# Kernel optimization log

Measured on AMD Instinct MI355X. Metric: run time of the kernel, lower is better.

Reference implementation:

```python
import jax, jax.numpy as jnp
import numpy as np

IN_CH = 32
HID = 2 * IN_CH          # 64
MASK_CH = 8 * 27         # 216


def conv3d(x, w, b, replicate_pad):
    # x: [B,C,D,H,W], w: [O,I,kd,kh,kw]
    if replicate_pad:
        x = jnp.pad(x, ((0, 0), (0, 0), (1, 1), (1, 1), (1, 1)), mode='edge')
    y = jax.lax.conv_general_dilated(
        x, w, window_strides=(1, 1, 1), padding='VALID',
        dimension_numbers=('NCDHW', 'OIDHW', 'NCDHW'))
    return y + b[None, :, None, None, None]


def unfold27(x):
    # replicate-padded 3x3x3 neighborhoods -> [B,C,D,H,W,27], n = kd*9+kh*3+kw
    B, C, D, H, W = x.shape
    xp = jnp.pad(x, ((0, 0), (0, 0), (1, 1), (1, 1), (1, 1)), mode='edge')
    patches = [xp[:, :, dz:dz + D, dy:dy + H, dx:dx + W]
               for dz in range(3) for dy in range(3) for dx in range(3)]
    return jnp.stack(patches, axis=-1)


def setup_inputs() -> dict:
    key = jax.random.key(0)
    ks = jax.random.split(key, 6)
    B, C, D, H, W = 1, IN_CH, 48, 48, 48
    x = jax.random.normal(ks[0], (B, C, D, H, W), dtype=jnp.float32)
    features = jax.random.normal(ks[1], (B, IN_CH, D, H, W), dtype=jnp.float32)
    # Conv(in, 2*in, k=3, replicate pad) ; Conv(2*in, 8*27, k=1, zeros pad)
    w1 = jax.random.normal(ks[2], (HID, IN_CH, 3, 3, 3), dtype=jnp.float32) * (1.0 / np.sqrt(IN_CH * 27))
    b1 = jnp.zeros((HID,), dtype=jnp.float32)
    w2 = jax.random.normal(ks[3], (MASK_CH, HID, 1, 1, 1), dtype=jnp.float32) * (1.0 / np.sqrt(HID))
    b2 = jnp.zeros((MASK_CH,), dtype=jnp.float32)
    return {"x": x, "features": features, "w1": w1, "b1": b1, "w2": w2, "b2": b2}


def reference(x, features, w1, b1, w2, b2):
    B, C, D, H, W = x.shape
    # mask network: Conv3 (replicate) -> SiLU -> Conv1 (zeros)
    h = jax.nn.silu(conv3d(features, w1, b1, replicate_pad=True))
    m = conv3d(h, w2, b2, replicate_pad=False)          # [B,216,D,H,W]
    # view(B,1,2,2,2,27,D,H,W).permute(0,1,6,2,7,3,8,4,5) -> [B,D,2,H,2,W,2,27]
    m = m.reshape(B, 2, 2, 2, 27, D, H, W)
    m = jnp.transpose(m, (0, 5, 1, 6, 2, 7, 3, 4))      # b d i h j w k n
    m = jax.nn.softmax(m, axis=-1)
    xu = unfold27(x)                                    # [B,C,D,H,W,27]
    # convex combination: contract over the 27 taps (batched small matmul)
    out = jnp.einsum('bdihjwkn,bcdhwn->bcdihjwk', m, xu)
    return out.reshape(B, C, 2 * D, 2 * H, 2 * W)
```

## Files before the change

kernel.cpp:

```cpp
#include <hip/hip_runtime.h>
#include <math.h>

#define NVOX 110592

typedef _Float16 f16x8 __attribute__((ext_vector_type(8)));
typedef _Float16 f16x4 __attribute__((ext_vector_type(4)));
typedef _Float16 f16x2 __attribute__((ext_vector_type(2)));
typedef float    f32x4 __attribute__((ext_vector_type(4)));

__device__ __forceinline__ void fmas4(float4& a, const float4& xv, float p) {
    a.x = fmaf(xv.x, p, a.x);
    a.y = fmaf(xv.y, p, a.y);
    a.z = fmaf(xv.z, p, a.z);
    a.w = fmaf(xv.w, p, a.w);
}
__device__ __forceinline__ float comp4(const float4& v, int j) {
    return j == 0 ? v.x : (j == 1 ? v.y : (j == 2 ? v.z : v.w));
}

__device__ __forceinline__ int xcd_swizzle(int bx, int nwg) {
    int chunk = nwg >> 3;
    return (bx & 7) * chunk + (bx >> 3);
}

__global__ void k_prep(const float* __restrict__ w1, const float* __restrict__ w2,
                       _Float16* __restrict__ w1h, _Float16* __restrict__ w2h) {
    int e = blockIdx.x * 256 + threadIdx.x;
    if (e < 64 * 32 * 27) {
        int oc = e / 864;
        int r = e - oc * 864;
        int ci = r / 27;
        int tap = r - ci * 27;
        w1h[oc * 864 + tap * 32 + ci] = (_Float16)w1[e];
    }
    int e2 = e - 55296;
    if (e2 >= 0 && e2 < 224 * 64) {
        int oc = e2 >> 6, k = e2 & 63;
        w2h[e2] = (oc < 216) ? (_Float16)w2[oc * 64 + k] : (_Float16)0.f;
    }
}

__global__ __launch_bounds__(256) void k_prepT(
    const float* __restrict__ feat, const float* __restrict__ x,
    _Float16* __restrict__ featT, _Float16* __restrict__ xT)
{
    __shared__ _Float16 tile[64 * 36];
    int bx = blockIdx.x;
    int which = bx >= 1728;
    int v0 = (which ? bx - 1728 : bx) * 64;
    const float* s = which ? x : feat;
    _Float16* dt = which ? xT : featT;
    int t = threadIdx.x;

    for (int i = t; i < 1024; i += 256) {
        int c2 = i >> 6, dv = i & 63;
        f16x2 v;
        v.x = (_Float16)s[(2 * c2) * NVOX + v0 + dv];
        v.y = (_Float16)s[(2 * c2 + 1) * NVOX + v0 + dv];
        *(f16x2*)(tile + dv * 36 + c2 * 2) = v;
    }
    __syncthreads();
    for (int i = t; i < 512; i += 256) {
        int dv = i >> 3, ch = i & 7;
        f16x4 v = *(const f16x4*)(tile + dv * 36 + ch * 4);
        *(f16x4*)(dt + (v0 + dv) * 32 + ch * 4) = v;
    }
}

__global__ __launch_bounds__(256, 4) void k_conv1(
    const _Float16* __restrict__ featT, const _Float16* __restrict__ w1h,
    const float* __restrict__ b1, _Float16* __restrict__ hout)
{
    __shared__ _Float16 flds[450 * 40];
    int bx = xcd_swizzle(blockIdx.x, gridDim.x);
    int d = bx / 48, hh = bx - d * 48;
    int t = threadIdx.x;

    for (int i = t; i < 1800; i += 256) {
        int col = i >> 2, chunk = i & 3;
        int dzdy = col / 50;
        int px = col - dzdy * 50;
        int dz = dzdy / 3, dy = dzdy - dz * 3;
        int zz = min(max(d + dz - 1, 0), 47);
        int yy = min(max(hh + dy - 1, 0), 47);
        int xx = min(max(px - 1, 0), 47);
        int vox = (zz * 48 + yy) * 48 + xx;
        *(f16x8*)(flds + col * 40 + chunk * 8) =
            *(const f16x8*)(featT + vox * 32 + chunk * 8);
    }
    __syncthreads();

    int wid = t >> 6;
    int lane = t & 63;
    int mcol = lane & 15;
    int q = lane >> 4;

    const _Float16* wbase = w1h + (wid * 16 + mcol) * 864 + q * 8;

    f32x4 acc0 = {0.f, 0.f, 0.f, 0.f};
    f32x4 acc1 = {0.f, 0.f, 0.f, 0.f};
    f32x4 acc2 = {0.f, 0.f, 0.f, 0.f};

#pragma unroll 3
    for (int dzdy = 0; dzdy < 9; ++dzdy) {
        const _Float16* brow = flds + (dzdy * 50 + mcol) * 40 + q * 8;
        const _Float16* wrow = wbase + dzdy * 96;
#pragma unroll
        for (int dx = 0; dx < 3; ++dx) {
            f16x8 av = *(const f16x8*)(wrow + dx * 32);
            const _Float16* bb = brow + dx * 40;
            f16x8 b0 = *(const f16x8*)(bb);
            f16x8 b1v = *(const f16x8*)(bb + 16 * 40);
            f16x8 b2v = *(const f16x8*)(bb + 32 * 40);
            acc0 = __builtin_amdgcn_mfma_f32_16x16x32_f16(av, b0, acc0, 0, 0, 0);
            acc1 = __builtin_amdgcn_mfma_f32_16x16x32_f16(av, b1v, acc1, 0, 0, 0);
            acc2 = __builtin_amdgcn_mfma_f32_16x16x32_f16(av, b2v, acc2, 0, 0, 0);
        }
    }

    __syncthreads();
    _Float16* transh = flds;
    float4 bv = ((const float4*)b1)[wid * 4 + q];
    {
        f32x4 accs[3] = {acc0, acc1, acc2};
#pragma unroll
        for (int p = 0; p < 3; ++p) {
            int px = p * 16 + mcol;
            f16x4 o;
            float s;
            s = accs[p][0] + bv.x; o.x = (_Float16)(s / (1.f + __expf(-s)));
            s = accs[p][1] + bv.y; o.y = (_Float16)(s / (1.f + __expf(-s)));
            s = accs[p][2] + bv.z; o.z = (_Float16)(s / (1.f + __expf(-s)));
            s = accs[p][3] + bv.w; o.w = (_Float16)(s / (1.f + __expf(-s)));
            *(f16x4*)(transh + px * 72 + wid * 16 + q * 4) = o;
        }
    }
    __syncthreads();
    for (int i = t; i < 384; i += 256) {
        int c = i & 7, px = i >> 3;
        f16x8 v = *(const f16x8*)(transh + px * 72 + c * 8);
        ((f16x8*)hout)[(bx * 48 + px) * 8 + c] = v;
    }
}

__global__ __launch_bounds__(256, 4) void k_fused(
    const _Float16* __restrict__ xT, const _Float16* __restrict__ hws,
    const _Float16* __restrict__ w2h, const float* __restrict__ b2,
    float* __restrict__ out)
{
    __shared__ float smem[10056];
    _Float16* hl = (_Float16*)(smem + 5376);
    _Float16* xh = (_Float16*)(smem + 5376);
    int bx = xcd_swizzle(blockIdx.x, gridDim.x);
    int d = bx / 96;
    int r = bx - d * 96;
    int hh = r >> 1;
    int w0 = (r & 1) * 24;
    int t = threadIdx.x;
    int vox0 = (d * 48 + hh) * 48 + w0;

    if (t < 192) {
        int vox = t >> 3, c = t & 7;
        *(f16x8*)(hl + vox * 72 + c * 8) = ((const f16x8*)hws)[(vox0 + vox) * 8 + c];
    } else {
        int i = t - 192;
        int vox = 24 + (i >> 3), c = i & 7;
        f16x8 z = {0, 0, 0, 0, 0, 0, 0, 0};
        *(f16x8*)(hl + vox * 72 + c * 8) = z;
    }
    __syncthreads();

    {
        int wid = t >> 6, lane = t & 63;
        int mcol = lane & 15, q = lane >> 4;
        for (int mt = wid; mt < 14; mt += 4) {
            float bias[4];
#pragma unroll
            for (int rr = 0; rr < 4; ++rr) {
                int oc = mt * 16 + q * 4 + rr;
                bias[rr] = (oc < 216) ? b2[oc] : 0.f;
            }
            f32x4 acc0 = {bias[0], bias[1], bias[2], bias[3]};
            f32x4 acc1 = acc0;
#pragma unroll
            for (int ks = 0; ks < 2; ++ks) {
                f16x8 av = *(const f16x8*)(w2h + (mt * 16 + mcol) * 64 + ks * 32 + q * 8);
                f16x8 bv0 = *(const f16x8*)(hl + mcol * 72 + ks * 32 + q * 8);
                f16x8 bv1 = *(const f16x8*)(hl + (16 + mcol) * 72 + ks * 32 + q * 8);
                acc0 = __builtin_amdgcn_mfma_f32_16x16x32_f16(av, bv0, acc0, 0, 0, 0);
                acc1 = __builtin_amdgcn_mfma_f32_16x16x32_f16(av, bv1, acc1, 0, 0, 0);
            }
#pragma unroll
            for (int rr = 0; rr < 4; ++rr) {
                int oc = mt * 16 + q * 4 + rr;
                if (oc < 216) {
                    int sub = oc / 27;
                    int n = oc - sub * 27;
                    smem[(sub * 24 + mcol) * 28 + n] = acc0[rr];
                    int vox1 = 16 + mcol;
                    if (vox1 < 24)
                        smem[(sub * 24 + vox1) * 28 + n] = acc1[rr];
                }
            }
        }
    }
    __syncthreads();

    for (int i = t; i < 936; i += 256) {
        int col = i >> 2, chunk = i & 3;
        int dzdy = col / 26;
        int px = col - dzdy * 26;
        int dz = dzdy / 3, dy = dzdy - dz * 3;
        int zz = min(max(d + dz - 1, 0), 47);
        int yy = min(max(hh + dy - 1, 0), 47);
        int xx = min(max(w0 + px - 1, 0), 47);
        int vox = (zz * 48 + yy) * 48 + xx;
        *(f16x8*)(xh + col * 40 + chunk * 8) =
            *(const f16x8*)(xT + vox * 32 + chunk * 8);
    }
    if (t < 192) {
        int sub = t / 24;
        int vox = t - sub * 24;
        float4* p4p = (float4*)(smem + (sub * 24 + vox) * 28);
        float4 v[7];
#pragma unroll
        for (int g = 0; g < 7; ++g) v[g] = p4p[g];
        float mx = fmaxf(fmaxf(v[6].x, v[6].y), v[6].z);
#pragma unroll
        for (int g = 0; g < 6; ++g)
            mx = fmaxf(mx, fmaxf(fmaxf(v[g].x, v[g].y), fmaxf(v[g].z, v[g].w)));
        float s = 0.f;
#pragma unroll
        for (int g = 0; g < 7; ++g) {
            v[g].x = __expf(v[g].x - mx);
            v[g].y = __expf(v[g].y - mx);
            v[g].z = __expf(v[g].z - mx);
            v[g].w = __expf(v[g].w - mx);
        }
        v[6].w = 0.f;
#pragma unroll
        for (int g = 0; g < 7; ++g) s += v[g].x + v[g].y + v[g].z + v[g].w;
        float inv = 1.f / s;
#pragma unroll
        for (int g = 0; g < 7; ++g) {
            v[g].x *= inv; v[g].y *= inv; v[g].z *= inv; v[g].w *= inv;
            p4p[g] = v[g];
        }
    }
    __syncthreads();

    float4* smem4 = (float4*)smem;
    int tx = t & 7, ty = t >> 3;
    int cq = ty & 7, sp = ty >> 3;
    float4 acc[2][3];
#pragma unroll
    for (int s = 0; s < 2; ++s)
#pragma unroll
        for (int wi = 0; wi < 3; ++wi)
            acc[s][wi] = make_float4(0.f, 0.f, 0.f, 0.f);

#pragma unroll
    for (int g = 0; g < 7; ++g) {
        float4 p4[2][3];
#pragma unroll
        for (int s = 0; s < 2; ++s)
#pragma unroll
            for (int wi = 0; wi < 3; ++wi)
                p4[s][wi] = smem4[((sp * 2 + s) * 24 + tx + wi * 8) * 7 + g];
#pragma unroll
        for (int j = 0; j < 4; ++j) {
            int n = g * 4 + j;
            if (n < 27) {
                int dz = n / 9;
                int rem = n - dz * 9;
                int dy = rem / 3, dx = rem - dy * 3;
#pragma unroll
                for (int wi = 0; wi < 3; ++wi) {
                    int col = (dz * 3 + dy) * 26 + tx + wi * 8 + dx;
                    f16x4 xr = *(const f16x4*)(xh + col * 40 + cq * 4);
                    float4 xv = make_float4((float)xr.x, (float)xr.y,
                                            (float)xr.z, (float)xr.w);
                    fmas4(acc[0][wi], xv, comp4(p4[0][wi], j));
                    fmas4(acc[1][wi], xv, comp4(p4[1][wi], j));
                }
            }
        }
    }

    int i_ = sp >> 1, j_ = sp & 1;
    int rowz = 2 * d + i_;
    int rowy = 2 * hh + j_;
#pragma unroll
    for (int wi = 0; wi < 3; ++wi) {
        int wg = w0 + tx + wi * 8;
#pragma unroll
        for (int cc = 0; cc < 4; ++cc) {
            int c = cq * 4 + cc;
            float2 v;
            v.x = comp4(acc[0][wi], cc);
            v.y = comp4(acc[1][wi], cc);
            *(float2*)(out + (((size_t)c * 96 + rowz) * 96 + rowy) * 96 + 2 * wg) = v;
        }
    }
}

extern "C" void kernel_launch(void* const* d_in, const int* in_sizes, int n_in,
                              void* d_out, int out_size, void* d_ws, size_t ws_size,
                              hipStream_t stream) {
    const float* x    = (const float*)d_in[0];
    const float* feat = (const float*)d_in[1];
    const float* w1   = (const float*)d_in[2];
    const float* b1   = (const float*)d_in[3];
    const float* w2   = (const float*)d_in[4];
    const float* b2   = (const float*)d_in[5];
    float* out = (float*)d_out;

    _Float16* w1h   = (_Float16*)d_ws;
    _Float16* w2h   = (_Float16*)((char*)d_ws + 110592);
    _Float16* featT = (_Float16*)((char*)d_ws + 139264);
    _Float16* xT    = (_Float16*)((char*)d_ws + 7217152);
    _Float16* hws   = (_Float16*)((char*)d_ws + 14295040);

    k_prep<<<272, 256, 0, stream>>>(w1, w2, w1h, w2h);
    k_prepT<<<3456, 256, 0, stream>>>(feat, x, featT, xT);
    k_conv1<<<2304, 256, 0, stream>>>(featT, w1h, b1, hws);
    k_fused<<<4608, 256, 0, stream>>>(xT, hws, w2h, b2, out);
}
```

Measured before the change: 258.9 us.

## Fuse conv1 with mask conv and softmax upsampling into one row kernel

```diff
diff --git a/kernel.cpp b/kernel.cpp
--- a/kernel.cpp
+++ b/kernel.cpp
@@ -23,34 +23,37 @@
     return (bx & 7) * chunk + (bx >> 3);
 }
 
-__global__ void k_prep(const float* __restrict__ w1, const float* __restrict__ w2,
-                       _Float16* __restrict__ w1h, _Float16* __restrict__ w2h) {
-    int e = blockIdx.x * 256 + threadIdx.x;
-    if (e < 64 * 32 * 27) {
-        int oc = e / 864;
-        int r = e - oc * 864;
-        int ci = r / 27;
-        int tap = r - ci * 27;
-        w1h[oc * 864 + tap * 32 + ci] = (_Float16)w1[e];
-    }
-    int e2 = e - 55296;
-    if (e2 >= 0 && e2 < 224 * 64) {
-        int oc = e2 >> 6, k = e2 & 63;
-        w2h[e2] = (oc < 216) ? (_Float16)w2[oc * 64 + k] : (_Float16)0.f;
-    }
-}
-
-__global__ __launch_bounds__(256) void k_prepT(
+__global__ __launch_bounds__(256) void k_prep(
     const float* __restrict__ feat, const float* __restrict__ x,
-    _Float16* __restrict__ featT, _Float16* __restrict__ xT)
+    const float* __restrict__ w1, const float* __restrict__ w2,
+    _Float16* __restrict__ featT, _Float16* __restrict__ xT,
+    _Float16* __restrict__ w1h, _Float16* __restrict__ w2h)
 {
     __shared__ _Float16 tile[64 * 36];
     int bx = blockIdx.x;
+    int t = threadIdx.x;
+
+    if (bx >= 3456) {
+        int e = (bx - 3456) * 256 + t;
+        if (e < 64 * 32 * 27) {
+            int oc = e / 864;
+            int r = e - oc * 864;
+            int ci = r / 27;
+            int tap = r - ci * 27;
+            w1h[oc * 864 + tap * 32 + ci] = (_Float16)w1[e];
+        }
+        int e2 = e - 55296;
+        if (e2 >= 0 && e2 < 224 * 64) {
+            int oc = e2 >> 6, k = e2 & 63;
+            w2h[e2] = (oc < 216) ? (_Float16)w2[oc * 64 + k] : (_Float16)0.f;
+        }
+        return;
+    }
+
     int which = bx >= 1728;
     int v0 = (which ? bx - 1728 : bx) * 64;
     const float* s = which ? x : feat;
     _Float16* dt = which ? xT : featT;
-    int t = threadIdx.x;
 
     for (int i = t; i < 1024; i += 256) {
         int c2 = i >> 6, dv = i & 63;
@@ -67,16 +70,22 @@
     }
 }
 
-__global__ __launch_bounds__(256, 4) void k_conv1(
-    const _Float16* __restrict__ featT, const _Float16* __restrict__ w1h,
-    const float* __restrict__ b1, _Float16* __restrict__ hout)
+__global__ __launch_bounds__(512, 4) void k_main(
+    const _Float16* __restrict__ featT, const _Float16* __restrict__ xT,
+    const _Float16* __restrict__ w1h, const float* __restrict__ b1,
+    const _Float16* __restrict__ w2h, const float* __restrict__ b2,
+    float* __restrict__ out)
 {
-    __shared__ _Float16 flds[450 * 40];
+    __shared__ float smem[19752];
+    float* mbuf = smem;
+    _Float16* X  = (_Float16*)(smem + 10752);
+    _Float16* hl = (_Float16*)(smem + 10752);
+
     int bx = xcd_swizzle(blockIdx.x, gridDim.x);
     int d = bx / 48, hh = bx - d * 48;
     int t = threadIdx.x;
 
-    for (int i = t; i < 1800; i += 256) {
+    for (int i = t; i < 1800; i += 512) {
         int col = i >> 2, chunk = i & 3;
         int dzdy = col / 50;
         int px = col - dzdy * 50;
@@ -85,7 +94,7 @@
         int yy = min(max(hh + dy - 1, 0), 47);
         int xx = min(max(px - 1, 0), 47);
         int vox = (zz * 48 + yy) * 48 + xx;
-        *(f16x8*)(flds + col * 40 + chunk * 8) =
+        *(f16x8*)(X + col * 40 + chunk * 8) =
             *(const f16x8*)(featT + vox * 32 + chunk * 8);
     }
     __syncthreads();
@@ -94,134 +103,99 @@
     int lane = t & 63;
     int mcol = lane & 15;
     int q = lane >> 4;
-
-    const _Float16* wbase = w1h + (wid * 16 + mcol) * 864 + q * 8;
-
-    f32x4 acc0 = {0.f, 0.f, 0.f, 0.f};
-    f32x4 acc1 = {0.f, 0.f, 0.f, 0.f};
-    f32x4 acc2 = {0.f, 0.f, 0.f, 0.f};
-
+    int ocs = wid & 3;
+
+    f32x4 c1a = {0.f, 0.f, 0.f, 0.f};
+    f32x4 c1b = {0.f, 0.f, 0.f, 0.f};
+    {
+        const _Float16* wbase = w1h + (ocs * 16 + mcol) * 864 + q * 8;
 #pragma unroll 3
-    for (int dzdy = 0; dzdy < 9; ++dzdy) {
-        const _Float16* brow = flds + (dzdy * 50 + mcol) * 40 + q * 8;
-        const _Float16* wrow = wbase + dzdy * 96;
-#pragma unroll
-        for (int dx = 0; dx < 3; ++dx) {
-            f16x8 av = *(const f16x8*)(wrow + dx * 32);
-            const _Float16* bb = brow + dx * 40;
-            f16x8 b0 = *(const f16x8*)(bb);
-            f16x8 b1v = *(const f16x8*)(bb + 16 * 40);
-            f16x8 b2v = *(const f16x8*)(bb + 32 * 40);
-            acc0 = __builtin_amdgcn_mfma_f32_16x16x32_f16(av, b0, acc0, 0, 0, 0);
-            acc1 = __builtin_amdgcn_mfma_f32_16x16x32_f16(av, b1v, acc1, 0, 0, 0);
-            acc2 = __builtin_amdgcn_mfma_f32_16x16x32_f16(av, b2v, acc2, 0, 0, 0);
-        }
-    }
-
-    __syncthreads();
-    _Float16* transh = flds;
-    float4 bv = ((const float4*)b1)[wid * 4 + q];
-    {
-        f32x4 accs[3] = {acc0, acc1, acc2};
-#pragma unroll
-        for (int p = 0; p < 3; ++p) {
-            int px = p * 16 + mcol;
-            f16x4 o;
-            float s;
-            s = accs[p][0] + bv.x; o.x = (_Float16)(s / (1.f + __expf(-s)));
-            s = accs[p][1] + bv.y; o.y = (_Float16)(s / (1.f + __expf(-s)));
-            s = accs[p][2] + bv.z; o.z = (_Float16)(s / (1.f + __expf(-s)));
-            s = accs[p][3] + bv.w; o.w = (_Float16)(s / (1.f + __expf(-s)));
-            *(f16x4*)(transh + px * 72 + wid * 16 + q * 4) = o;
-        }
-    }
-    __syncthreads();
-    for (int i = t; i < 384; i += 256) {
-        int c = i & 7, px = i >> 3;
-        f16x8 v = *(const f16x8*)(transh + px * 72 + c * 8);
-        ((f16x8*)hout)[(bx * 48 + px) * 8 + c] = v;
-    }
-}
-
-__global__ __launch_bounds__(256, 4) void k_fused(
-    const _Float16* __restrict__ xT, const _Float16* __restrict__ hws,
-    const _Float16* __restrict__ w2h, const float* __restrict__ b2,
-    float* __restrict__ out)
-{
-    __shared__ float smem[10056];
-    _Float16* hl = (_Float16*)(smem + 5376);
-    _Float16* xh = (_Float16*)(smem + 5376);
-    int bx = xcd_swizzle(blockIdx.x, gridDim.x);
-    int d = bx / 96;
-    int r = bx - d * 96;
-    int hh = r >> 1;
-    int w0 = (r & 1) * 24;
-    int t = threadIdx.x;
-    int vox0 = (d * 48 + hh) * 48 + w0;
-
-    if (t < 192) {
-        int vox = t >> 3, c = t & 7;
-        *(f16x8*)(hl + vox * 72 + c * 8) = ((const f16x8*)hws)[(vox0 + vox) * 8 + c];
-    } else {
-        int i = t - 192;
-        int vox = 24 + (i >> 3), c = i & 7;
-        f16x8 z = {0, 0, 0, 0, 0, 0, 0, 0};
-        *(f16x8*)(hl + vox * 72 + c * 8) = z;
-    }
-    __syncthreads();
-
-    {
-        int wid = t >> 6, lane = t & 63;
-        int mcol = lane & 15, q = lane >> 4;
-        for (int mt = wid; mt < 14; mt += 4) {
-            float bias[4];
-#pragma unroll
-            for (int rr = 0; rr < 4; ++rr) {
-                int oc = mt * 16 + q * 4 + rr;
-                bias[rr] = (oc < 216) ? b2[oc] : 0.f;
-            }
-            f32x4 acc0 = {bias[0], bias[1], bias[2], bias[3]};
-            f32x4 acc1 = acc0;
-#pragma unroll
-            for (int ks = 0; ks < 2; ++ks) {
-                f16x8 av = *(const f16x8*)(w2h + (mt * 16 + mcol) * 64 + ks * 32 + q * 8);
-                f16x8 bv0 = *(const f16x8*)(hl + mcol * 72 + ks * 32 + q * 8);
-                f16x8 bv1 = *(const f16x8*)(hl + (16 + mcol) * 72 + ks * 32 + q * 8);
-                acc0 = __builtin_amdgcn_mfma_f32_16x16x32_f16(av, bv0, acc0, 0, 0, 0);
-                acc1 = __builtin_amdgcn_mfma_f32_16x16x32_f16(av, bv1, acc1, 0, 0, 0);
-            }
-#pragma unroll
-            for (int rr = 0; rr < 4; ++rr) {
-                int oc = mt * 16 + q * 4 + rr;
-                if (oc < 216) {
-                    int sub = oc / 27;
-                    int n = oc - sub * 27;
-                    smem[(sub * 24 + mcol) * 28 + n] = acc0[rr];
-                    int vox1 = 16 + mcol;
-                    if (vox1 < 24)
-                        smem[(sub * 24 + vox1) * 28 + n] = acc1[rr];
+        for (int dzdy = 0; dzdy < 9; ++dzdy) {
+            const _Float16* brow = X + (dzdy * 50 + mcol) * 40 + q * 8;
+            const _Float16* wrow = wbase + dzdy * 96;
+#pragma unroll
+            for (int dx = 0; dx < 3; ++dx) {
+                f16x8 av = *(const f16x8*)(wrow + dx * 32);
+                const _Float16* bb = brow + dx * 40;
+                if (wid < 4) {
+                    f16x8 b0 = *(const f16x8*)(bb);
+                    f16x8 b2v = *(const f16x8*)(bb + 32 * 40);
+                    c1a = __builtin_amdgcn_mfma_f32_16x16x32_f16(av, b0, c1a, 0, 0, 0);
+                    c1b = __builtin_amdgcn_mfma_f32_16x16x32_f16(av, b2v, c1b, 0, 0, 0);
+                } else {
+                    f16x8 b1v = *(const f16x8*)(bb + 16 * 40);
+                    c1a = __builtin_amdgcn_mfma_f32_16x16x32_f16(av, b1v, c1a, 0, 0, 0);
                 }
             }
         }
     }
     __syncthreads();
 
-    for (int i = t; i < 936; i += 256) {
+    {
+        float4 bv = ((const float4*)b1)[ocs * 4 + q];
+        int pxb0 = (wid < 4) ? 0 : 1;
+        int px0 = pxb0 * 16 + mcol;
+        f16x4 o; float s;
+        s = c1a[0] + bv.x; o.x = (_Float16)(s / (1.f + __expf(-s)));
+        s = c1a[1] + bv.y; o.y = (_Float16)(s / (1.f + __expf(-s)));
+        s = c1a[2] + bv.z; o.z = (_Float16)(s / (1.f + __expf(-s)));
+        s = c1a[3] + bv.w; o.w = (_Float16)(s / (1.f + __expf(-s)));
+        *(f16x4*)(hl + px0 * 72 + ocs * 16 + q * 4) = o;
+        if (wid < 4) {
+            int px1 = 32 + mcol;
+            s = c1b[0] + bv.x; o.x = (_Float16)(s / (1.f + __expf(-s)));
+            s = c1b[1] + bv.y; o.y = (_Float16)(s / (1.f + __expf(-s)));
+            s = c1b[2] + bv.z; o.z = (_Float16)(s / (1.f + __expf(-s)));
+            s = c1b[3] + bv.w; o.w = (_Float16)(s / (1.f + __expf(-s)));
+            *(f16x4*)(hl + px1 * 72 + ocs * 16 + q * 4) = o;
+        }
+    }
+    __syncthreads();
+
+    for (int tt = wid; tt < 42; tt += 8) {
+        int mt = tt / 3, nt = tt - mt * 3;
+        float bias[4];
+#pragma unroll
+        for (int rr = 0; rr < 4; ++rr) {
+            int oc = mt * 16 + q * 4 + rr;
+            bias[rr] = (oc < 216) ? b2[oc] : 0.f;
+        }
+        f32x4 acc = {bias[0], bias[1], bias[2], bias[3]};
+#pragma unroll
+        for (int ks = 0; ks < 2; ++ks) {
+            f16x8 av = *(const f16x8*)(w2h + (mt * 16 + mcol) * 64 + ks * 32 + q * 8);
+            f16x8 bv = *(const f16x8*)(hl + (nt * 16 + mcol) * 72 + ks * 32 + q * 8);
+            acc = __builtin_amdgcn_mfma_f32_16x16x32_f16(av, bv, acc, 0, 0, 0);
+        }
+        int vox = nt * 16 + mcol;
+#pragma unroll
+        for (int rr = 0; rr < 4; ++rr) {
+            int oc = mt * 16 + q * 4 + rr;
+            if (oc < 216) {
+                int sub = oc / 27;
+                int n = oc - sub * 27;
+                mbuf[(sub * 48 + vox) * 28 + n] = acc[rr];
+            }
+        }
+    }
+    __syncthreads();
+
+    for (int i = t; i < 1800; i += 512) {
         int col = i >> 2, chunk = i & 3;
-        int dzdy = col / 26;
-        int px = col - dzdy * 26;
+        int dzdy = col / 50;
+        int px = col - dzdy * 50;
         int dz = dzdy / 3, dy = dzdy - dz * 3;
         int zz = min(max(d + dz - 1, 0), 47);
         int yy = min(max(hh + dy - 1, 0), 47);
-        int xx = min(max(w0 + px - 1, 0), 47);
+        int xx = min(max(px - 1, 0), 47);
         int vox = (zz * 48 + yy) * 48 + xx;
-        *(f16x8*)(xh + col * 40 + chunk * 8) =
+        *(f16x8*)(X + col * 40 + chunk * 8) =
             *(const f16x8*)(xT + vox * 32 + chunk * 8);
     }
-    if (t < 192) {
-        int sub = t / 24;
-        int vox = t - sub * 24;
-        float4* p4p = (float4*)(smem + (sub * 24 + vox) * 28);
+    if (t < 384) {
+        int sub = t / 48;
+        int vox = t - sub * 48;
+        float4* p4p = (float4*)(mbuf + (sub * 48 + vox) * 28);
         float4 v[7];
 #pragma unroll
         for (int g = 0; g < 7; ++g) v[g] = p4p[g];
@@ -250,7 +224,10 @@
     __syncthreads();
 
     float4* smem4 = (float4*)smem;
-    int tx = t & 7, ty = t >> 3;
+    int u = t & 255;
+    int half = t >> 8;
+    int w0 = half * 24;
+    int tx = u & 7, ty = u >> 3;
     int cq = ty & 7, sp = ty >> 3;
     float4 acc[2][3];
 #pragma unroll
@@ -266,7 +243,7 @@
         for (int s = 0; s < 2; ++s)
 #pragma unroll
             for (int wi = 0; wi < 3; ++wi)
-                p4[s][wi] = smem4[((sp * 2 + s) * 24 + tx + wi * 8) * 7 + g];
+                p4[s][wi] = smem4[((sp * 2 + s) * 48 + w0 + tx + wi * 8) * 7 + g];
 #pragma unroll
         for (int j = 0; j < 4; ++j) {
             int n = g * 4 + j;
@@ -276,8 +253,8 @@
                 int dy = rem / 3, dx = rem - dy * 3;
 #pragma unroll
                 for (int wi = 0; wi < 3; ++wi) {
-                    int col = (dz * 3 + dy) * 26 + tx + wi * 8 + dx;
-                    f16x4 xr = *(const f16x4*)(xh + col * 40 + cq * 4);
+                    int col = (dz * 3 + dy) * 50 + w0 + tx + wi * 8 + dx;
+                    f16x4 xr = *(const f16x4*)(X + col * 40 + cq * 4);
                     float4 xv = make_float4((float)xr.x, (float)xr.y,
                                             (float)xr.z, (float)xr.w);
                     fmas4(acc[0][wi], xv, comp4(p4[0][wi], j));
@@ -319,10 +296,7 @@
     _Float16* w2h   = (_Float16*)((char*)d_ws + 110592);
     _Float16* featT = (_Float16*)((char*)d_ws + 139264);
     _Float16* xT    = (_Float16*)((char*)d_ws + 7217152);
-    _Float16* hws   = (_Float16*)((char*)d_ws + 14295040);
-
-    k_prep<<<272, 256, 0, stream>>>(w1, w2, w1h, w2h);
-    k_prepT<<<3456, 256, 0, stream>>>(feat, x, featT, xT);
-    k_conv1<<<2304, 256, 0, stream>>>(featT, w1h, b1, hws);
-    k_fused<<<4608, 256, 0, stream>>>(xT, hws, w2h, b2, out);
-}
+
+    k_prep<<<3728, 256, 0, stream>>>(feat, x, w1, w2, featT, xT, w1h, w2h);
+    k_main<<<2304, 512, 0, stream>>>(featT, xT, w1h, b1, w2h, b2, out);
+}
```

Result: faster. 247.6 us (-4.4%).
